# Kernel optimization log

Measured on AMD Instinct MI355X. Metric: run time of the kernel, lower is better.

The kernel has to match this reference:

```python
import jax, jax.numpy as jnp
import numpy as np

D = 768
SCALE = 1.0 / np.sqrt(D)  # 1/sqrt(question_size)
NEG_INF = -1e30


def setup_inputs() -> dict:
    key = jax.random.key(0)
    k1, k2, k3, k4 = jax.random.split(key, 4)
    B, Lc, Lq = 8, 2048, 1024
    context_hiddens = jax.random.normal(k1, (B, Lc, D), dtype=jnp.float32)
    context_mask = jnp.ones((B, Lc), dtype=jnp.float32)  # unused by forward (parity with original)
    question_hiddens = jax.random.normal(k2, (B, Lq, D), dtype=jnp.float32)
    question_mask = jax.random.randint(k3, (B, Lq), 0, 2, dtype=jnp.int32)
    # ensure at least one valid question token per row to avoid all -inf softmax
    question_mask = question_mask.at[:, 0].set(1)
    W = jax.random.normal(k4, (D, D), dtype=jnp.float32) * (1.0 / np.sqrt(D))
    b = jnp.zeros((D,), dtype=jnp.float32)
    return {
        "context_hiddens": context_hiddens,
        "context_mask": context_mask,
        "question_hiddens": question_hiddens,
        "question_mask": question_mask,
        "W": W,
        "b": b,
    }


def reference(context_hiddens, context_mask, question_hiddens, question_mask, W, b):
    # Linear projection of question hiddens: [B, Lq, D]
    query = jnp.einsum("bqd,ed->bqe", question_hiddens, W) + b
    # Bilinear scores: c_i' W q_j -> [B, Lc, Lq], scaled
    scores = jnp.einsum("bcd,bqd->bcq", context_hiddens, query) * SCALE
    # Masked softmax over question axis (mask==1 means valid)
    mask = question_mask[:, None, :].astype(jnp.bool_)  # [B, 1, Lq]
    scores = jnp.where(mask, scores, NEG_INF)
    attention_dist = jax.nn.softmax(scores, axis=2)
    # Weighted sum of question hiddens: [B, Lc, D]
    attn_output = jnp.einsum("bcq,bqd->bcd", attention_dist, question_hiddens)
    return jnp.concatenate([context_hiddens, attn_output], axis=2)  # [B, Lc, 2D]
```

## Files before the change

### kernel.cpp

```cpp
#include <hip/hip_runtime.h>
#include <hip/hip_bf16.h>
#include <cstdint>
#include <cstddef>

#define D 768
#define BATCH 8
#define LC 2048
#define LQ 1024
#define SCALE 0.03608439182435161f

typedef __attribute__((ext_vector_type(8))) short short8;
typedef __attribute__((ext_vector_type(4))) float floatx4;

__device__ __forceinline__ short f2bf(float f) {
    union { float f; uint32_t u; } v; v.f = f;
    uint32_t r = v.u + 0x7fffu + ((v.u >> 16) & 1u);
    return (short)(r >> 16);
}

__device__ __forceinline__ void gl_lds16(const short* g, short* l) {
    __builtin_amdgcn_global_load_lds(
        reinterpret_cast<const __attribute__((address_space(1))) unsigned int*>(
            reinterpret_cast<uintptr_t>(g)),
        reinterpret_cast<__attribute__((address_space(3))) unsigned int*>(
            reinterpret_cast<uintptr_t>(l)),
        16, 0, 0);
}

__device__ __forceinline__ void gemm128x256_loop(
    const short* __restrict__ A, const short* __restrict__ B,
    int lda, int ldb, int K, int m0, int n0,
    short* lds, int tid, floatx4 acc[4][4]) {
    const int lane = tid & 63, l15 = lane & 15, quad = lane >> 4;
    const int w = tid >> 6, wm = w >> 2, wn = w & 3;

    const int ra = tid >> 2, sa = (tid & 3) ^ (ra & 3);
    const short* gA = A + (size_t)(m0 + ra) * lda + sa * 8;
    short* dA = lds + tid * 8;
    const int cb0 = tid, cb1 = tid + 512;
    const int rb0 = cb0 >> 2, sb0 = (cb0 & 3) ^ (rb0 & 3);
    const int rb1 = cb1 >> 2, sb1 = (cb1 & 3) ^ (rb1 & 3);
    const short* gB0 = B + (size_t)(n0 + rb0) * ldb + sb0 * 8;
    const short* gB1 = B + (size_t)(n0 + rb1) * ldb + sb1 * 8;
    short* dB0 = lds + 4096 + cb0 * 8;
    short* dB1 = lds + 4096 + cb1 * 8;

    int aoff[4], boff[4];
#pragma unroll
    for (int mt = 0; mt < 4; ++mt) {
        int r = wm * 64 + mt * 16 + l15;
        aoff[mt] = r * 32 + ((quad ^ (r & 3)) * 8);
    }
#pragma unroll
    for (int nt = 0; nt < 4; ++nt) {
        int r = wn * 64 + nt * 16 + l15;
        boff[nt] = 4096 + r * 32 + ((quad ^ (r & 3)) * 8);
    }

    const int NT = K >> 5;
#define STAGE_A(t, bb) { gl_lds16(gA + (t) * 32, dA + (bb)); }
#define STAGE_B(t, bb) { gl_lds16(gB0 + (t) * 32, dB0 + (bb)); gl_lds16(gB1 + (t) * 32, dB1 + (bb)); }
    STAGE_A(0, 0) STAGE_B(0, 0)
    STAGE_A(1, 12288) STAGE_B(1, 12288)

    for (int kt = 0; kt < NT; ++kt) {
        const int cur = (kt % 3) * 12288;
        const int nxt = ((kt + 2) % 3) * 12288;
        if (kt + 1 < NT) { asm volatile("s_waitcnt vmcnt(3)" ::: "memory"); }
        else             { asm volatile("s_waitcnt vmcnt(0)" ::: "memory"); }
        __builtin_amdgcn_s_barrier();
        __builtin_amdgcn_sched_barrier(0);

        if (kt + 2 < NT) STAGE_A((kt + 2), nxt)

        short8 af[4], bf[4];
#pragma unroll
        for (int mt = 0; mt < 4; ++mt)
            af[mt] = *reinterpret_cast<const short8*>(lds + cur + aoff[mt]);
#pragma unroll
        for (int nt = 0; nt < 2; ++nt)
            bf[nt] = *reinterpret_cast<const short8*>(lds + cur + boff[nt]);
        __builtin_amdgcn_s_setprio(1);
#pragma unroll
        for (int mt = 0; mt < 4; ++mt)
#pragma unroll
            for (int nt = 0; nt < 2; ++nt)
                acc[mt][nt] = __builtin_amdgcn_mfma_f32_16x16x32_bf16(af[mt], bf[nt], acc[mt][nt], 0, 0, 0);
        __builtin_amdgcn_s_setprio(0);

        if (kt + 2 < NT) STAGE_B((kt + 2), nxt)

#pragma unroll
        for (int nt = 2; nt < 4; ++nt)
            bf[nt] = *reinterpret_cast<const short8*>(lds + cur + boff[nt]);
        __builtin_amdgcn_s_setprio(1);
#pragma unroll
        for (int mt = 0; mt < 4; ++mt)
#pragma unroll
            for (int nt = 2; nt < 4; ++nt)
                acc[mt][nt] = __builtin_amdgcn_mfma_f32_16x16x32_bf16(af[mt], bf[nt], acc[mt][nt], 0, 0, 0);
        __builtin_amdgcn_s_setprio(0);
        __builtin_amdgcn_sched_barrier(0);
    }
#undef STAGE_A
#undef STAGE_B
}

__global__ __launch_bounds__(256) void prep_kernel(
    const float* __restrict__ ctx, const float* __restrict__ qh,
    const float* __restrict__ Wf, float* __restrict__ out,
    short* __restrict__ W_b, short* __restrict__ ctx_b,
    short* __restrict__ qh_b, short* __restrict__ qhT, float* __restrict__ sums) {
    __shared__ float tile[32][33];
    const int tid = threadIdx.x;
    const int bid = blockIdx.x;
    const int gid = bid * 256 + tid;

    if (gid < 147456) {
        float4 v = reinterpret_cast<const float4*>(Wf)[gid];
        short4 o;
        o.x = f2bf(v.x); o.y = f2bf(v.y); o.z = f2bf(v.z); o.w = f2bf(v.w);
        reinterpret_cast<short4*>(W_b)[gid] = o;
    }
    if (gid < 4096) {
        float4 z = {0.f, 0.f, 0.f, 0.f};
        reinterpret_cast<float4*>(sums)[gid] = z;
    }
#pragma unroll
    for (int it = 0; it < 6; ++it) {
        int i = gid + it * 524288;
        int row = i / 192, c4 = i % 192;
        float4 v = reinterpret_cast<const float4*>(ctx)[i];
        reinterpret_cast<float4*>(out)[(size_t)row * 384 + c4] = v;
        short4 o;
        o.x = f2bf(v.x); o.y = f2bf(v.y); o.z = f2bf(v.z); o.w = f2bf(v.w);
        reinterpret_cast<short4*>(ctx_b)[i] = o;
    }
    const int r = tid >> 3, c = (tid & 7) * 4;
#pragma unroll
    for (int it = 0; it < 3; ++it) {
        const int T = bid + it * 2048;
        const int b = T / 768, rem = T % 768;
        const int q0 = (rem / 24) * 32, d0 = (rem % 24) * 32;
        const float4 v = *reinterpret_cast<const float4*>(
            qh + ((size_t)b * LQ + q0 + r) * D + d0 + c);
        tile[r][c] = v.x; tile[r][c + 1] = v.y; tile[r][c + 2] = v.z; tile[r][c + 3] = v.w;
        short4 d;
        d.x = f2bf(v.x); d.y = f2bf(v.y); d.z = f2bf(v.z); d.w = f2bf(v.w);
        *reinterpret_cast<short4*>(qh_b + ((size_t)b * LQ + q0 + r) * D + d0 + c) = d;
        __syncthreads();
        short4 o;
        o.x = f2bf(tile[c][r]); o.y = f2bf(tile[c + 1][r]);
        o.z = f2bf(tile[c + 2][r]); o.w = f2bf(tile[c + 3][r]);
        *reinterpret_cast<short4*>(qhT + ((size_t)b * D + d0 + r) * LQ + q0 + c) = o;
        __syncthreads();
    }
}

__global__ __launch_bounds__(512, 4) void gemm1_kernel(
    const short* __restrict__ A, const short* __restrict__ W,
    const float* __restrict__ bias, short* __restrict__ Q) {
    __shared__ __align__(16) short lds[3 * 12288];
    const int nb = (blockIdx.x & 7) * 24 + (blockIdx.x >> 3);
    const int m0 = (nb / 3) * 128, n0 = (nb % 3) * 256;
    const int tid = threadIdx.x;
    const int lane = tid & 63, l15 = lane & 15, quad = lane >> 4;
    const int w = tid >> 6, wm = w >> 2, wn = w & 3;
    floatx4 acc[4][4];
#pragma unroll
    for (int i = 0; i < 4; ++i)
#pragma unroll
        for (int j = 0; j < 4; ++j) { floatx4 z = {0.f, 0.f, 0.f, 0.f}; acc[i][j] = z; }
    gemm128x256_loop(A, W, D, D, D, m0, n0, lds, tid, acc);
    float bv[4];
#pragma unroll
    for (int nt = 0; nt < 4; ++nt) bv[nt] = bias[n0 + wn * 64 + nt * 16 + l15];
#pragma unroll
    for (int mt = 0; mt < 4; ++mt)
#pragma unroll
        for (int rr = 0; rr < 4; ++rr) {
            int row = m0 + wm * 64 + mt * 16 + quad * 4 + rr;
#pragma unroll
            for (int nt = 0; nt < 4; ++nt)
                Q[(size_t)row * D + n0 + wn * 64 + nt * 16 + l15] = f2bf(acc[mt][nt][rr] + bv[nt]);
        }
}

__global__ __launch_bounds__(512, 4) void scores_kernel(
    const short* __restrict__ ctxb, const short* __restrict__ query_b,
    const int* __restrict__ qmask, short* __restrict__ P, float* __restrict__ sums) {
    __shared__ __align__(16) short lds[3 * 12288];
    const int nb = ((blockIdx.x & 7) << 6) + (blockIdx.x >> 3);
    const int b = nb >> 6, rem = nb & 63, bx = rem >> 2, by = rem & 3;
    const int m0 = bx << 7, n0 = by << 8;
    const int tid = threadIdx.x;
    const int lane = tid & 63, l15 = lane & 15, quad = lane >> 4;
    const int w = tid >> 6, wm = w >> 2, wn = w & 3;
    floatx4 acc[4][4];
#pragma unroll
    for (int i = 0; i < 4; ++i)
#pragma unroll
        for (int j = 0; j < 4; ++j) { floatx4 z = {0.f, 0.f, 0.f, 0.f}; acc[i][j] = z; }
    gemm128x256_loop(ctxb + (size_t)b * LC * D, query_b + (size_t)b * LQ * D,
                     D, D, D, m0, n0, lds, tid, acc);
    const int* mk = qmask + b * LQ;
    bool valid[4];
#pragma unroll
    for (int nt = 0; nt < 4; ++nt) valid[nt] = (mk[n0 + wn * 64 + nt * 16 + l15] != 0);
    short* Pb = P + (size_t)b * LC * LQ;
    float* sumb = sums + (size_t)b * LC;
#pragma unroll
    for (int mt = 0; mt < 4; ++mt)
#pragma unroll
        for (int rr = 0; rr < 4; ++rr) {
            int row = m0 + wm * 64 + mt * 16 + quad * 4 + rr;
            float psum = 0.f;
#pragma unroll
            for (int nt = 0; nt < 4; ++nt) {
                float pv = valid[nt] ? __expf(acc[mt][nt][rr] * SCALE) : 0.f;
                psum += pv;
                Pb[(size_t)row * LQ + n0 + wn * 64 + nt * 16 + l15] = f2bf(pv);
            }
#pragma unroll
            for (int off = 1; off < 16; off <<= 1)
                psum += __shfl_xor(psum, off, 64);
            if (l15 == 0)
                atomicAdd(&sumb[row], psum);
        }
}

__global__ __launch_bounds__(512, 4) void gemm2_kernel(
    const short* __restrict__ P, const short* __restrict__ qhT,
    const float* __restrict__ sums, float* __restrict__ out) {
    __shared__ __align__(16) short lds[3 * 12288];
    const int nb = (blockIdx.x & 7) * 48 + (blockIdx.x >> 3);
    const int b = nb / 48, rem = nb % 48, bx = rem / 3, by = rem % 3;
    const int m0 = bx << 7, n0 = by << 8;
    const int tid = threadIdx.x;
    const int lane = tid & 63, l15 = lane & 15, quad = lane >> 4;
    const int w = tid >> 6, wm = w >> 2, wn = w & 3;
    floatx4 acc[4][4];
#pragma unroll
    for (int i = 0; i < 4; ++i)
#pragma unroll
        for (int j = 0; j < 4; ++j) { floatx4 z = {0.f, 0.f, 0.f, 0.f}; acc[i][j] = z; }
    gemm128x256_loop(P + (size_t)b * LC * LQ, qhT + (size_t)b * D * LQ,
                     LQ, LQ, LQ, m0, n0, lds, tid, acc);
    const float* sumb = sums + (size_t)b * LC;
#pragma unroll
    for (int mt = 0; mt < 4; ++mt)
#pragma unroll
        for (int rr = 0; rr < 4; ++rr) {
            int lrow = m0 + wm * 64 + mt * 16 + quad * 4 + rr;
            const float inv = 1.0f / sumb[lrow];
            size_t rowoff = ((size_t)b * LC + lrow) * 1536 + 768;
#pragma unroll
            for (int nt = 0; nt < 4; ++nt)
                out[rowoff + n0 + wn * 64 + nt * 16 + l15] = acc[mt][nt][rr] * inv;
        }
}

extern "C" void kernel_launch(void* const* d_in, const int* in_sizes, int n_in,
                              void* d_out, int out_size, void* d_ws, size_t ws_size,
                              hipStream_t stream) {
    const float* ctx = (const float*)d_in[0];
    const float* qh = (const float*)d_in[2];
    const int* qmask = (const int*)d_in[3];
    const float* Wf = (const float*)d_in[4];
    const float* bias = (const float*)d_in[5];
    float* out = (float*)d_out;

    char* ws = (char*)d_ws;
    short* W_b     = (short*)(ws);
    short* query_b = (short*)(ws + 1179648);
    short* qhT     = (short*)(ws + 13762560);
    short* ctx_b   = (short*)(ws + 26345472);
    short* P       = (short*)(ws + 51511296);
    float* sums    = (float*)(ws + 85065728);
    short* qh_b    = (short*)(ws + 51511296);

    prep_kernel<<<2048, 256, 0, stream>>>(ctx, qh, Wf, out, W_b, ctx_b, qh_b, qhT, sums);
    gemm1_kernel<<<192, 512, 0, stream>>>(qh_b, W_b, bias, query_b);
    scores_kernel<<<512, 512, 0, stream>>>(ctx_b, query_b, qmask, P, sums);
    gemm2_kernel<<<384, 512, 0, stream>>>(P, qhT, sums, out);
}
```

Baseline: 269.2 us.

## Fuse scores and PV GEMMs into a flash-style attention kernel

Replaces the separate scores kernel, which wrote the bf16 probability matrix P to global memory with atomic row sums, and the second GEMM kernel with one fused kernel. Each block holds a 64-row context tile in LDS, computes 128-column score chunks, exponentiates them into an LDS P tile, and accumulates P times the transposed question hiddens in registers. Row sums are reduced in shared memory, so the global P round trip, the sums buffer and the atomics go away. In exchange, the B operands (query and qhT) are read straight from global memory with no LDS staging, only 256 blocks are launched, and register pressure from 24 accumulator tiles is high.

```diff
diff --git a/kernel.cpp b/kernel.cpp
--- a/kernel.cpp
+++ b/kernel.cpp
@@ -110,7 +110,7 @@
     const float* __restrict__ ctx, const float* __restrict__ qh,
     const float* __restrict__ Wf, float* __restrict__ out,
     short* __restrict__ W_b, short* __restrict__ ctx_b,
-    short* __restrict__ qh_b, short* __restrict__ qhT, float* __restrict__ sums) {
+    short* __restrict__ qh_b, short* __restrict__ qhT) {
     __shared__ float tile[32][33];
     const int tid = threadIdx.x;
     const int bid = blockIdx.x;
@@ -121,10 +121,6 @@
         short4 o;
         o.x = f2bf(v.x); o.y = f2bf(v.y); o.z = f2bf(v.z); o.w = f2bf(v.w);
         reinterpret_cast<short4*>(W_b)[gid] = o;
-    }
-    if (gid < 4096) {
-        float4 z = {0.f, 0.f, 0.f, 0.f};
-        reinterpret_cast<float4*>(sums)[gid] = z;
     }
 #pragma unroll
     for (int it = 0; it < 6; ++it) {
@@ -186,77 +182,131 @@
         }
 }
 
-__global__ __launch_bounds__(512, 4) void scores_kernel(
+#define CTXS 49152
+__global__ __launch_bounds__(512, 2) void attn_kernel(
     const short* __restrict__ ctxb, const short* __restrict__ query_b,
-    const int* __restrict__ qmask, short* __restrict__ P, float* __restrict__ sums) {
-    __shared__ __align__(16) short lds[3 * 12288];
-    const int nb = ((blockIdx.x & 7) << 6) + (blockIdx.x >> 3);
-    const int b = nb >> 6, rem = nb & 63, bx = rem >> 2, by = rem & 3;
-    const int m0 = bx << 7, n0 = by << 8;
+    const short* __restrict__ qhT, const int* __restrict__ qmask,
+    float* __restrict__ out) {
+    __shared__ __align__(16) short lds[CTXS + 8192];
+    __shared__ float rowsum4[4][64];
     const int tid = threadIdx.x;
+    const int b = blockIdx.x & 7;
+    const int rowblk = blockIdx.x >> 3;
+    const int m0 = rowblk * 64;
     const int lane = tid & 63, l15 = lane & 15, quad = lane >> 4;
     const int w = tid >> 6, wm = w >> 2, wn = w & 3;
-    floatx4 acc[4][4];
-#pragma unroll
-    for (int i = 0; i < 4; ++i)
-#pragma unroll
-        for (int j = 0; j < 4; ++j) { floatx4 z = {0.f, 0.f, 0.f, 0.f}; acc[i][j] = z; }
-    gemm128x256_loop(ctxb + (size_t)b * LC * D, query_b + (size_t)b * LQ * D,
-                     D, D, D, m0, n0, lds, tid, acc);
+
+    const short* cbase = ctxb + ((size_t)b * LC + m0) * D;
+#pragma unroll
+    for (int i = 0; i < 12; ++i) {
+        int cch = tid + i * 512;
+        int row = cch / 96, s = cch - row * 96;
+        gl_lds16(cbase + (size_t)row * D + ((s ^ (row & 7)) * 8), lds + cch * 8);
+    }
+
+    int abase[2], axor[2], pabase[2];
+#pragma unroll
+    for (int mt = 0; mt < 2; ++mt) {
+        int ar = wm * 32 + mt * 16 + l15;
+        abase[mt] = ar * 768; axor[mt] = ar & 7;
+        pabase[mt] = CTXS + ar * 128;
+    }
+    const short* qb = query_b + (size_t)b * LQ * D + (size_t)(wn * 32 + l15) * D + quad * 8;
+    const short* qt = qhT + (size_t)b * D * LQ + (size_t)(wn * 192 + l15) * LQ + quad * 8;
     const int* mk = qmask + b * LQ;
-    bool valid[4];
-#pragma unroll
-    for (int nt = 0; nt < 4; ++nt) valid[nt] = (mk[n0 + wn * 64 + nt * 16 + l15] != 0);
-    short* Pb = P + (size_t)b * LC * LQ;
-    float* sumb = sums + (size_t)b * LC;
-#pragma unroll
-    for (int mt = 0; mt < 4; ++mt)
+
+    floatx4 oacc[2][12];
+#pragma unroll
+    for (int i = 0; i < 2; ++i)
+#pragma unroll
+        for (int j = 0; j < 12; ++j) { floatx4 z = {0.f, 0.f, 0.f, 0.f}; oacc[i][j] = z; }
+    float psum[2][4];
+#pragma unroll
+    for (int i = 0; i < 2; ++i)
+#pragma unroll
+        for (int j = 0; j < 4; ++j) psum[i][j] = 0.f;
+
+    asm volatile("s_waitcnt vmcnt(0)" ::: "memory");
+    __builtin_amdgcn_s_barrier();
+
+    for (int ch = 0; ch < 8; ++ch) {
+        const int q0 = ch * 128;
+        floatx4 sacc[2][2];
+#pragma unroll
+        for (int i = 0; i < 2; ++i)
+#pragma unroll
+            for (int j = 0; j < 2; ++j) { floatx4 z = {0.f, 0.f, 0.f, 0.f}; sacc[i][j] = z; }
+        const short* qbc = qb + (size_t)q0 * D;
+#pragma unroll 8
+        for (int kt = 0; kt < 24; ++kt) {
+            short8 bf0 = *reinterpret_cast<const short8*>(qbc + kt * 32);
+            short8 bf1 = *reinterpret_cast<const short8*>(qbc + 16 * D + kt * 32);
+            short8 af0 = *reinterpret_cast<const short8*>(lds + abase[0] + ((kt * 4 + quad) ^ axor[0]) * 8);
+            short8 af1 = *reinterpret_cast<const short8*>(lds + abase[1] + ((kt * 4 + quad) ^ axor[1]) * 8);
+            sacc[0][0] = __builtin_amdgcn_mfma_f32_16x16x32_bf16(af0, bf0, sacc[0][0], 0, 0, 0);
+            sacc[0][1] = __builtin_amdgcn_mfma_f32_16x16x32_bf16(af0, bf1, sacc[0][1], 0, 0, 0);
+            sacc[1][0] = __builtin_amdgcn_mfma_f32_16x16x32_bf16(af1, bf0, sacc[1][0], 0, 0, 0);
+            sacc[1][1] = __builtin_amdgcn_mfma_f32_16x16x32_bf16(af1, bf1, sacc[1][1], 0, 0, 0);
+        }
+        bool valid0 = (mk[q0 + wn * 32 + l15] != 0);
+        bool valid1 = (mk[q0 + wn * 32 + 16 + l15] != 0);
+#pragma unroll
+        for (int mt = 0; mt < 2; ++mt)
+#pragma unroll
+            for (int rr = 0; rr < 4; ++rr) {
+                int prow = wm * 32 + mt * 16 + quad * 4 + rr;
+                float pv0 = valid0 ? __expf(sacc[mt][0][rr] * SCALE) : 0.f;
+                float pv1 = valid1 ? __expf(sacc[mt][1][rr] * SCALE) : 0.f;
+                int pc0 = wn * 32 + l15;
+                int pc1 = pc0 + 16;
+                lds[CTXS + prow * 128 + ((((pc0 >> 3) ^ (prow & 7)) << 3) | (pc0 & 7))] = f2bf(pv0);
+                lds[CTXS + prow * 128 + ((((pc1 >> 3) ^ (prow & 7)) << 3) | (pc1 & 7))] = f2bf(pv1);
+                float rsum = pv0 + pv1;
+#pragma unroll
+                for (int off = 1; off < 16; off <<= 1)
+                    rsum += __shfl_xor(rsum, off, 64);
+                psum[mt][rr] += rsum;
+            }
+        asm volatile("s_waitcnt lgkmcnt(0)" ::: "memory");
+        __builtin_amdgcn_sched_barrier(0);
+        __builtin_amdgcn_s_barrier();
+        __builtin_amdgcn_sched_barrier(0);
+        const short* qtc = qt + q0;
+#pragma unroll
+        for (int kt = 0; kt < 4; ++kt) {
+            short8 pa0 = *reinterpret_cast<const short8*>(lds + pabase[0] + ((kt * 4 + quad) ^ axor[0]) * 8);
+            short8 pa1 = *reinterpret_cast<const short8*>(lds + pabase[1] + ((kt * 4 + quad) ^ axor[1]) * 8);
+#pragma unroll
+            for (int nt = 0; nt < 12; ++nt) {
+                short8 bq = *reinterpret_cast<const short8*>(qtc + (size_t)nt * 16 * LQ + kt * 32);
+                oacc[0][nt] = __builtin_amdgcn_mfma_f32_16x16x32_bf16(pa0, bq, oacc[0][nt], 0, 0, 0);
+                oacc[1][nt] = __builtin_amdgcn_mfma_f32_16x16x32_bf16(pa1, bq, oacc[1][nt], 0, 0, 0);
+            }
+        }
+        __builtin_amdgcn_sched_barrier(0);
+        __builtin_amdgcn_s_barrier();
+        __builtin_amdgcn_sched_barrier(0);
+    }
+    if (l15 == 0) {
+#pragma unroll
+        for (int mt = 0; mt < 2; ++mt)
+#pragma unroll
+            for (int rr = 0; rr < 4; ++rr)
+                rowsum4[wn][wm * 32 + mt * 16 + quad * 4 + rr] = psum[mt][rr];
+    }
+    __syncthreads();
+#pragma unroll
+    for (int mt = 0; mt < 2; ++mt)
 #pragma unroll
         for (int rr = 0; rr < 4; ++rr) {
-            int row = m0 + wm * 64 + mt * 16 + quad * 4 + rr;
-            float psum = 0.f;
-#pragma unroll
-            for (int nt = 0; nt < 4; ++nt) {
-                float pv = valid[nt] ? __expf(acc[mt][nt][rr] * SCALE) : 0.f;
-                psum += pv;
-                Pb[(size_t)row * LQ + n0 + wn * 64 + nt * 16 + l15] = f2bf(pv);
-            }
-#pragma unroll
-            for (int off = 1; off < 16; off <<= 1)
-                psum += __shfl_xor(psum, off, 64);
-            if (l15 == 0)
-                atomicAdd(&sumb[row], psum);
-        }
-}
-
-__global__ __launch_bounds__(512, 4) void gemm2_kernel(
-    const short* __restrict__ P, const short* __restrict__ qhT,
-    const float* __restrict__ sums, float* __restrict__ out) {
-    __shared__ __align__(16) short lds[3 * 12288];
-    const int nb = (blockIdx.x & 7) * 48 + (blockIdx.x >> 3);
-    const int b = nb / 48, rem = nb % 48, bx = rem / 3, by = rem % 3;
-    const int m0 = bx << 7, n0 = by << 8;
-    const int tid = threadIdx.x;
-    const int lane = tid & 63, l15 = lane & 15, quad = lane >> 4;
-    const int w = tid >> 6, wm = w >> 2, wn = w & 3;
-    floatx4 acc[4][4];
-#pragma unroll
-    for (int i = 0; i < 4; ++i)
-#pragma unroll
-        for (int j = 0; j < 4; ++j) { floatx4 z = {0.f, 0.f, 0.f, 0.f}; acc[i][j] = z; }
-    gemm128x256_loop(P + (size_t)b * LC * LQ, qhT + (size_t)b * D * LQ,
-                     LQ, LQ, LQ, m0, n0, lds, tid, acc);
-    const float* sumb = sums + (size_t)b * LC;
-#pragma unroll
-    for (int mt = 0; mt < 4; ++mt)
-#pragma unroll
-        for (int rr = 0; rr < 4; ++rr) {
-            int lrow = m0 + wm * 64 + mt * 16 + quad * 4 + rr;
-            const float inv = 1.0f / sumb[lrow];
-            size_t rowoff = ((size_t)b * LC + lrow) * 1536 + 768;
-#pragma unroll
-            for (int nt = 0; nt < 4; ++nt)
-                out[rowoff + n0 + wn * 64 + nt * 16 + l15] = acc[mt][nt][rr] * inv;
+            int prow = wm * 32 + mt * 16 + quad * 4 + rr;
+            int lrow = m0 + prow;
+            const float inv = 1.0f / (rowsum4[0][prow] + rowsum4[1][prow] +
+                                      rowsum4[2][prow] + rowsum4[3][prow]);
+            size_t ro = ((size_t)b * LC + lrow) * 1536 + 768;
+#pragma unroll
+            for (int nt = 0; nt < 12; ++nt)
+                out[ro + wn * 192 + nt * 16 + l15] = oacc[mt][nt][rr] * inv;
         }
 }
 
@@ -275,12 +325,9 @@
     short* query_b = (short*)(ws + 1179648);
     short* qhT     = (short*)(ws + 13762560);
     short* ctx_b   = (short*)(ws + 26345472);
-    short* P       = (short*)(ws + 51511296);
-    float* sums    = (float*)(ws + 85065728);
     short* qh_b    = (short*)(ws + 51511296);
 
-    prep_kernel<<<2048, 256, 0, stream>>>(ctx, qh, Wf, out, W_b, ctx_b, qh_b, qhT, sums);
+    prep_kernel<<<2048, 256, 0, stream>>>(ctx, qh, Wf, out, W_b, ctx_b, qh_b, qhT);
     gemm1_kernel<<<192, 512, 0, stream>>>(qh_b, W_b, bias, query_b);
-    scores_kernel<<<512, 512, 0, stream>>>(ctx_b, query_b, qmask, P, sums);
-    gemm2_kernel<<<384, 512, 0, stream>>>(P, qhT, sums, out);
-}
+    attn_kernel<<<256, 512, 0, stream>>>(ctx_b, query_b, qhT, qmask, out);
+}
```

Result: slower. 390.9 us (+45.2%).
